# Optimization experiments

Hardware: AMD Instinct MI355X
Metric: run time of the kernel (lower is better)

The kernel has to match this reference:

```python
import jax, jax.numpy as jnp
import numpy as np

B, N, C, H, P, K = 32, 4096, 64, 256, 8, 2


def setup_inputs() -> dict:
    key = jax.random.key(0)
    k1, k2, k3, k4 = jax.random.split(key, 4)
    s1 = 1.0 / np.sqrt(C)
    s2 = 1.0 / np.sqrt(H)
    return {
        "u_t": jax.random.normal(k1, (B, N, C), dtype=jnp.float32),
        "W1": jax.random.normal(k2, (P, C, H), dtype=jnp.float32) * s1,
        "b1": jnp.zeros((P, H), dtype=jnp.float32),
        "W2": jax.random.normal(k3, (P, H, C), dtype=jnp.float32) * s2,
        "b2": jnp.zeros((P, C), dtype=jnp.float32),
        "Wr": jax.random.normal(k4, (C, P), dtype=jnp.float32) * s1,
        "br": jnp.zeros((P,), dtype=jnp.float32),
        "top_k": K,
    }


def reference(u_t, W1, b1, W2, b2, Wr, br, top_k):
    # u_state = u_t[..., :output_channels]; here C_in == output_channels
    u_state = u_t
    # Router: mean-pool over spatial points -> per-sample logits over primitives
    pooled = jnp.mean(u_state, axis=1)                     # (B, C)
    logits = pooled @ Wr + br                              # (B, P)
    topk_vals, topk_idx = jax.lax.top_k(logits, top_k)     # (B, K)
    w = jax.nn.softmax(topk_vals, axis=-1)                 # (B, K) combine weights
    # Sparse dispatch: gather only the selected experts' params per sample
    W1e = W1[topk_idx]                                     # (B, K, C, H)
    b1e = b1[topk_idx]                                     # (B, K, H)
    W2e = W2[topk_idx]                                     # (B, K, H, C)
    b2e = b2[topk_idx]                                     # (B, K, C)
    # Primitive operator: pointwise 2-layer GELU MLP (erf gelu, torch default)
    h1 = jax.nn.gelu(jnp.einsum('bnc,bkch->bknh', u_t, W1e) + b1e[:, :, None, :],
                     approximate=False)                    # (B, K, N, H)
    delta = jnp.einsum('bknh,bkhc->bknc', h1, W2e) + b2e[:, :, None, :]  # (B, K, N, C)
    # Weighted combine: delta_sum = sum_k w_k * delta_k
    delta_sum = jnp.einsum('bknc,bk->bnc', delta, w)       # (B, N, C)
    return u_state + delta_sum
```

## Files before the change

### kernel.cpp

```cpp
#include <hip/hip_runtime.h>
#include <hip/hip_bf16.h>
#include <math.h>

#define B_ 32
#define N_ 4096
#define C_ 64
#define H_ 256
#define P_ 8
#define NPOOL 1024

typedef short bf16x8 __attribute__((ext_vector_type(8)));
typedef float f32x4 __attribute__((ext_vector_type(4)));

union BF8 { bf16x8 v; unsigned int w[4]; };

__device__ __forceinline__ unsigned short f2bf(float f) {
    union { float f; unsigned int u; } v; v.f = f;
    unsigned int r = v.u + 0x7FFFu + ((v.u >> 16) & 1u);
    return (unsigned short)(r >> 16);
}
__device__ __forceinline__ float bf2f(unsigned short h) {
    union { float f; unsigned int u; } v; v.u = ((unsigned int)h) << 16; return v.f;
}
__device__ __forceinline__ unsigned int pk_bf16(float lo, float hi) {
    unsigned int r;
    asm("v_cvt_pk_bf16_f32 %0, %1, %2" : "=v"(r) : "v"(lo), "v"(hi));
    return r;
}
__device__ __forceinline__ float gelu_w(float x, float wk) {
    float x2 = x * x;
    float y2 = x * fmaf(0.10294322f, x2, 2.30220772f);
    float e  = __builtin_amdgcn_exp2f(y2);
    float rc = __builtin_amdgcn_rcpf(e + 1.0f);
    float wx = wk * x;
    return fmaf(-wx, rc, wx);
}
__device__ __forceinline__ int hperm_p(int p) {
    int t = p >> 4, d = p & 15;
    return ((t >> 1) << 5) + ((d >> 2) << 3) + ((t & 1) << 2) + (d & 3);
}

__global__ void prep_pool(const float* __restrict__ W1, const float* __restrict__ W2,
                          const float* __restrict__ b1, const float* __restrict__ u,
                          const float* __restrict__ Wr, const float* __restrict__ br,
                          unsigned short* __restrict__ W1P, unsigned short* __restrict__ W2T,
                          unsigned short* __restrict__ b1P, float* __restrict__ pooled,
                          int* __restrict__ counter, float4* __restrict__ route) {
    __shared__ union {
        unsigned short t[256 * 66];
        unsigned short s[64 * 258];
        struct { float red[4][64]; float lgAll[B_][P_]; } pr;
    } sh;
    __shared__ int isLast;

    const int bid = blockIdx.x, tid = threadIdx.x;

    if (bid < 16) {
        const int e = bid >> 1, m = bid & 1;
        if (m == 0) {
            const float* src = W1 + (e << 14);
            #pragma unroll
            for (int i = 0; i < 16; ++i) {
                int c = i * 4 + (tid >> 6), h4 = (tid & 63) * 4;
                float4 v = *(const float4*)(src + c * 256 + h4);
                sh.t[(h4 + 0) * 66 + c] = f2bf(v.x);
                sh.t[(h4 + 1) * 66 + c] = f2bf(v.y);
                sh.t[(h4 + 2) * 66 + c] = f2bf(v.z);
                sh.t[(h4 + 3) * 66 + c] = f2bf(v.w);
            }
            __syncthreads();
            unsigned short* dst = W1P + (e << 14);
            #pragma unroll
            for (int i = 0; i < 32; ++i) {
                int p = i * 8 + (tid >> 5), c2 = (tid & 31) * 2;
                int h = hperm_p(p);
                *(ushort2*)(dst + (p << 6) + c2) = *(const ushort2*)&sh.t[h * 66 + c2];
            }
        } else {
            const float* src = W2 + (e << 14);
            #pragma unroll
            for (int i = 0; i < 16; ++i) {
                int h = i * 16 + (tid >> 4), c4 = (tid & 15) * 4;
                float4 v = *(const float4*)(src + (h << 6) + c4);
                sh.s[(c4 + 0) * 258 + h] = f2bf(v.x);
                sh.s[(c4 + 1) * 258 + h] = f2bf(v.y);
                sh.s[(c4 + 2) * 258 + h] = f2bf(v.z);
                sh.s[(c4 + 3) * 258 + h] = f2bf(v.w);
            }
            __syncthreads();
            unsigned short* dst = W2T + (e << 14);
            #pragma unroll
            for (int i = 0; i < 32; ++i) {
                int c = i * 2 + (tid >> 7), h2 = (tid & 127) * 2;
                *(ushort2*)(dst + (c << 8) + h2) = *(const ushort2*)&sh.s[c * 258 + h2];
            }
        }
        return;
    }
    if (bid == 16) {
        #pragma unroll
        for (int i = 0; i < 8; ++i) {
            int oi = i * 256 + tid;
            int e = oi >> 8, p = oi & 255;
            b1P[oi] = f2bf(b1[(e << 8) + hperm_p(p)]);
        }
        return;
    }
    int pb = bid - 17;
    int b = pb >> 5, chunk = pb & 31;
    int c = tid & 63, rg = tid >> 6;
    const float* base = u + ((size_t)b * N_ + (size_t)chunk * 128) * C_;
    float s = 0.f;
    #pragma unroll 4
    for (int i = 0; i < 32; ++i) s += base[(i * 4 + rg) * C_ + c];
    sh.pr.red[rg][c] = s;
    __syncthreads();
    if (tid < 64) {
        float t4 = sh.pr.red[0][tid] + sh.pr.red[1][tid] + sh.pr.red[2][tid] + sh.pr.red[3][tid];
        atomicAdd(&pooled[b * C_ + tid], t4);
        __threadfence();
    }
    __syncthreads();
    if (tid == 0) {
        int old = atomicAdd(counter, 1);
        isLast = (old == NPOOL - 1);
    }
    __syncthreads();
    if (!isLast) return;
    __threadfence();
    {
        int rb = tid >> 3, p = tid & 7;
        const float* pb2 = pooled + rb * C_;
        float sacc = br[p];
        #pragma unroll
        for (int cc = 0; cc < C_; ++cc) {
            float pv = __hip_atomic_load(&pb2[cc], __ATOMIC_RELAXED, __HIP_MEMORY_SCOPE_AGENT);
            sacc += pv * (1.0f / N_) * Wr[cc * P_ + p];
        }
        sh.pr.lgAll[rb][p] = sacc;
    }
    __syncthreads();
    if (tid < B_) {
        float lg[P_];
        #pragma unroll
        for (int p = 0; p < P_; ++p) lg[p] = sh.pr.lgAll[tid][p];
        int i0 = 0;
        #pragma unroll
        for (int p = 1; p < P_; ++p) if (lg[p] > lg[i0]) i0 = p;
        int i1 = (i0 == 0) ? 1 : 0;
        #pragma unroll
        for (int p = 0; p < P_; ++p) if (p != i0 && lg[p] > lg[i1]) i1 = p;
        float e1 = __expf(lg[i1] - lg[i0]);
        float w0 = 1.f / (1.f + e1);
        route[tid] = make_float4(w0, e1 * w0, __int_as_float(i0), __int_as_float(i1));
    }
}

__device__ __forceinline__ void comp_tp(const bf16x8 (&A)[2][2], const bf16x8 (&Bw)[4],
                                        ushort4 bva, ushort4 bvb, float wk,
                                        const bf16x8 (&ub)[4][2], f32x4 (&acc2)[4][4]) {
    f32x4 c1[2][4];
    #pragma unroll
    for (int tt = 0; tt < 2; ++tt)
        #pragma unroll
        for (int rt = 0; rt < 4; ++rt)
            #pragma unroll
            for (int q = 0; q < 4; ++q) c1[tt][rt][q] = 0.f;
    #pragma unroll
    for (int ks = 0; ks < 2; ++ks)
        #pragma unroll
        for (int tt = 0; tt < 2; ++tt)
            #pragma unroll
            for (int rt = 0; rt < 4; ++rt)
                c1[tt][rt] = __builtin_amdgcn_mfma_f32_16x16x32_bf16(A[tt][ks], ub[rt][ks], c1[tt][rt], 0, 0, 0);
    float bv[8];
    bv[0] = bf2f(bva.x); bv[1] = bf2f(bva.y); bv[2] = bf2f(bva.z); bv[3] = bf2f(bva.w);
    bv[4] = bf2f(bvb.x); bv[5] = bf2f(bvb.y); bv[6] = bf2f(bvb.z); bv[7] = bf2f(bvb.w);
    #pragma unroll
    for (int rt = 0; rt < 4; ++rt) {
        float gv[8];
        #pragma unroll
        for (int j = 0; j < 4; ++j) {
            gv[j]     = gelu_w(c1[0][rt][j] + bv[j],     wk);
            gv[4 + j] = gelu_w(c1[1][rt][j] + bv[4 + j], wk);
        }
        BF8 t;
        t.w[0] = pk_bf16(gv[0], gv[1]); t.w[1] = pk_bf16(gv[2], gv[3]);
        t.w[2] = pk_bf16(gv[4], gv[5]); t.w[3] = pk_bf16(gv[6], gv[7]);
        bf16x8 a2 = t.v;
        #pragma unroll
        for (int ct = 0; ct < 4; ++ct)
            acc2[ct][rt] = __builtin_amdgcn_mfma_f32_16x16x32_bf16(a2, Bw[ct], acc2[ct][rt], 0, 0, 0);
    }
}

#define LOADS(A, Bw, bva, bvb, tp) \
    A[0][0] = *(const bf16x8*)(w1p + (((tp) * 32 +  0 + r) << 6) +  0 + g * 8); \
    A[0][1] = *(const bf16x8*)(w1p + (((tp) * 32 +  0 + r) << 6) + 32 + g * 8); \
    A[1][0] = *(const bf16x8*)(w1p + (((tp) * 32 + 16 + r) << 6) +  0 + g * 8); \
    A[1][1] = *(const bf16x8*)(w1p + (((tp) * 32 + 16 + r) << 6) + 32 + g * 8); \
    Bw[0] = *(const bf16x8*)(w2t + (( 0 + r) << 8) + (tp) * 32 + g * 8); \
    Bw[1] = *(const bf16x8*)(w2t + ((16 + r) << 8) + (tp) * 32 + g * 8); \
    Bw[2] = *(const bf16x8*)(w2t + ((32 + r) << 8) + (tp) * 32 + g * 8); \
    Bw[3] = *(const bf16x8*)(w2t + ((48 + r) << 8) + (tp) * 32 + g * 8); \
    bva = *(const ushort4*)(b1e + (tp) * 32 + 4 * g); \
    bvb = *(const ushort4*)(b1e + (tp) * 32 + 16 + 4 * g);

__global__ __launch_bounds__(256, 2)
void moe_main(const float* __restrict__ u, const unsigned short* __restrict__ W1P,
              const unsigned short* __restrict__ W2T, const unsigned short* __restrict__ b1P,
              const float* __restrict__ b2, const float4* __restrict__ route,
              float* __restrict__ out) {
    const int tid = threadIdx.x;
    const int wv = tid >> 6, lane = tid & 63;
    const int r = lane & 15, g = lane >> 4;
    const int b = blockIdx.x >> 4;
    const int nslab = ((blockIdx.x & 15) << 2) + wv;
    const int n0 = nslab << 6;

    float4 rd = route[b];

    const float* ubase = u + ((size_t)b * N_ + n0) * C_;
    bf16x8 ub[4][2];
    #pragma unroll
    for (int rt = 0; rt < 4; ++rt) {
        const float* rp = ubase + (rt * 16 + r) * C_;
        #pragma unroll
        for (int ks = 0; ks < 2; ++ks) {
            float4 lo = *(const float4*)(rp + ks * 32 + g * 8);
            float4 hi = *(const float4*)(rp + ks * 32 + g * 8 + 4);
            BF8 t;
            t.w[0] = pk_bf16(lo.x, lo.y); t.w[1] = pk_bf16(lo.z, lo.w);
            t.w[2] = pk_bf16(hi.x, hi.y); t.w[3] = pk_bf16(hi.z, hi.w);
            ub[rt][ks] = t.v;
        }
    }

    f32x4 acc2[4][4];
    #pragma unroll
    for (int ct = 0; ct < 4; ++ct)
        #pragma unroll
        for (int rt = 0; rt < 4; ++rt)
            #pragma unroll
            for (int q = 0; q < 4; ++q) acc2[ct][rt][q] = 0.f;

    #pragma unroll
    for (int ke = 0; ke < 2; ++ke) {
        const int e = ke ? __float_as_int(rd.w) : __float_as_int(rd.z);
        const float wk = ke ? rd.y : rd.x;
        const unsigned short* w1p = W1P + (e << 14);
        const unsigned short* w2t = W2T + (e << 14);
        const unsigned short* b1e = b1P + (e << 8);

        bf16x8 Aa[2][2], Ba[4]; ushort4 va0, va1;
        bf16x8 Ab[2][2], Bb[4]; ushort4 vb0, vb1;
        LOADS(Aa, Ba, va0, va1, 0)
        #pragma unroll
        for (int tpp = 0; tpp < 4; ++tpp) {
            LOADS(Ab, Bb, vb0, vb1, 2 * tpp + 1)
            comp_tp(Aa, Ba, va0, va1, wk, ub, acc2);
            if (tpp < 3) { LOADS(Aa, Ba, va0, va1, 2 * tpp + 2) }
            comp_tp(Ab, Bb, vb0, vb1, wk, ub, acc2);
        }
    }

    const int e0 = __float_as_int(rd.z), e1i = __float_as_int(rd.w);
    float bsum[4];
    #pragma unroll
    for (int ct = 0; ct < 4; ++ct) {
        int c = ct * 16 + r;
        bsum[ct] = rd.x * b2[e0 * C_ + c] + rd.y * b2[e1i * C_ + c];
    }
    float* obase = out + ((size_t)b * N_ + n0) * C_;
    #pragma unroll
    for (int rt = 0; rt < 4; ++rt)
        #pragma unroll
        for (int j = 0; j < 4; ++j) {
            int row = rt * 16 + 4 * g + j;
            #pragma unroll
            for (int ct = 0; ct < 4; ++ct) {
                int c = ct * 16 + r;
                obase[row * C_ + c] = ubase[row * C_ + c] + acc2[ct][rt][j] + bsum[ct];
            }
        }
}

extern "C" void kernel_launch(void* const* d_in, const int* in_sizes, int n_in,
                              void* d_out, int out_size, void* d_ws, size_t ws_size,
                              hipStream_t stream) {
    const float* u  = (const float*)d_in[0];
    const float* W1 = (const float*)d_in[1];
    const float* b1 = (const float*)d_in[2];
    const float* W2 = (const float*)d_in[3];
    const float* b2 = (const float*)d_in[4];
    const float* Wr = (const float*)d_in[5];
    const float* br = (const float*)d_in[6];
    float* out = (float*)d_out;

    char* ws = (char*)d_ws;
    float* pooled        = (float*)ws;
    int* counter         = (int*)(ws + 8192);
    float4* route        = (float4*)(ws + 8256);
    unsigned short* b1P  = (unsigned short*)(ws + 8768);
    unsigned short* W1P  = (unsigned short*)(ws + 16384);
    unsigned short* W2T  = (unsigned short*)(ws + 16384 + 262144);

    hipMemsetAsync(ws, 0, 8256, stream);
    prep_pool<<<1041, 256, 0, stream>>>(W1, W2, b1, u, Wr, br, W1P, W2T, b1P, pooled, counter, route);
    moe_main<<<512, 256, 0, stream>>>(u, W1P, W2T, b1P, b2, route, out);
}
```

Baseline: 171.3 us.

## Stage expert weights into LDS via direct global-to-LDS loads in fragment layout

The prep kernel now writes each expert's W1, W2 and b1 into one contiguous block already laid out in MFMA fragment order, folding the separate bias block into the weight-conversion blocks. The main kernel copies the selected expert's block into shared memory with global_load_lds and reads fragments from LDS instead of issuing per-wave global loads. The b1 bias is folded into the MFMA accumulator initialisation. This removes the four-fold redundant global and L2 weight traffic across waves, but adds about 64KB of LDS per block, which may limit occupancy to two blocks per CU. It also adds block-wide barriers and removes the register double-buffered prefetch overlap.

```diff
diff --git a/kernel.cpp b/kernel.cpp
--- a/kernel.cpp
+++ b/kernel.cpp
@@ -8,11 +8,12 @@
 #define H_ 256
 #define P_ 8
 #define NPOOL 1024
+#define EBLK 66048
 
 typedef short bf16x8 __attribute__((ext_vector_type(8)));
 typedef float f32x4 __attribute__((ext_vector_type(4)));
 
-union BF8 { bf16x8 v; unsigned int w[4]; };
+union BF8 { bf16x8 v; unsigned int w[4]; unsigned short h[8]; };
 
 __device__ __forceinline__ unsigned short f2bf(float f) {
     union { float f; unsigned int u; } v; v.f = f;
@@ -39,12 +40,16 @@
     int t = p >> 4, d = p & 15;
     return ((t >> 1) << 5) + ((d >> 2) << 3) + ((t & 1) << 2) + (d & 3);
 }
+__device__ __forceinline__ void gload16(const void* g, void* l) {
+    __builtin_amdgcn_global_load_lds(
+        (const __attribute__((address_space(1))) unsigned int*)g,
+        (__attribute__((address_space(3))) unsigned int*)l, 16, 0, 0);
+}
 
 __global__ void prep_pool(const float* __restrict__ W1, const float* __restrict__ W2,
                           const float* __restrict__ b1, const float* __restrict__ u,
                           const float* __restrict__ Wr, const float* __restrict__ br,
-                          unsigned short* __restrict__ W1P, unsigned short* __restrict__ W2T,
-                          unsigned short* __restrict__ b1P, float* __restrict__ pooled,
+                          unsigned short* __restrict__ WL, float* __restrict__ pooled,
                           int* __restrict__ counter, float4* __restrict__ route) {
     __shared__ union {
         unsigned short t[256 * 66];
@@ -57,6 +62,7 @@
 
     if (bid < 16) {
         const int e = bid >> 1, m = bid & 1;
+        unsigned short* dstW = WL + (size_t)e * (EBLK / 2);
         if (m == 0) {
             const float* src = W1 + (e << 14);
             #pragma unroll
@@ -69,12 +75,24 @@
                 sh.t[(h4 + 3) * 66 + c] = f2bf(v.w);
             }
             __syncthreads();
-            unsigned short* dst = W1P + (e << 14);
-            #pragma unroll
-            for (int i = 0; i < 32; ++i) {
-                int p = i * 8 + (tid >> 5), c2 = (tid & 31) * 2;
-                int h = hperm_p(p);
-                *(ushort2*)(dst + (p << 6) + c2) = *(const ushort2*)&sh.t[h * 66 + c2];
+            #pragma unroll
+            for (int i = 0; i < 8; ++i) {
+                int idx = i * 256 + tid;
+                int fid = idx >> 6, ln = idx & 63;
+                int tp = fid >> 2, tt = (fid >> 1) & 1, ks = fid & 1;
+                int rr = ln & 15, gg = ln >> 4;
+                const unsigned short* sp = &sh.t[hperm_p(tp * 32 + tt * 16 + rr) * 66 + ks * 32 + gg * 8];
+                BF8 o;
+                #pragma unroll
+                for (int mm = 0; mm < 8; ++mm) o.h[mm] = sp[mm];
+                *(bf16x8*)(dstW + ((fid * 64 + ln) << 3)) = o.v;
+            }
+            if (tid < 32) {
+                BF8 o;
+                #pragma unroll
+                for (int mm = 0; mm < 8; ++mm)
+                    o.h[mm] = f2bf(b1[(e << 8) + hperm_p(tid * 8 + mm)]);
+                *(bf16x8*)(dstW + 32768 + (tid << 3)) = o.v;
             }
         } else {
             const float* src = W2 + (e << 14);
@@ -88,25 +106,22 @@
                 sh.s[(c4 + 3) * 258 + h] = f2bf(v.w);
             }
             __syncthreads();
-            unsigned short* dst = W2T + (e << 14);
-            #pragma unroll
-            for (int i = 0; i < 32; ++i) {
-                int c = i * 2 + (tid >> 7), h2 = (tid & 127) * 2;
-                *(ushort2*)(dst + (c << 8) + h2) = *(const ushort2*)&sh.s[c * 258 + h2];
+            #pragma unroll
+            for (int i = 0; i < 8; ++i) {
+                int idx = i * 256 + tid;
+                int fid = idx >> 6, ln = idx & 63;
+                int tp = fid >> 2, ct = fid & 3;
+                int rr = ln & 15, gg = ln >> 4;
+                const unsigned short* sp = &sh.s[(ct * 16 + rr) * 258 + tp * 32 + gg * 8];
+                BF8 o;
+                #pragma unroll
+                for (int mm = 0; mm < 8; ++mm) o.h[mm] = sp[mm];
+                *(bf16x8*)(dstW + 16384 + ((fid * 64 + ln) << 3)) = o.v;
             }
         }
         return;
     }
-    if (bid == 16) {
-        #pragma unroll
-        for (int i = 0; i < 8; ++i) {
-            int oi = i * 256 + tid;
-            int e = oi >> 8, p = oi & 255;
-            b1P[oi] = f2bf(b1[(e << 8) + hperm_p(p)]);
-        }
-        return;
-    }
-    int pb = bid - 17;
+    int pb = bid - 16;
     int b = pb >> 5, chunk = pb & 31;
     int c = tid & 63, rg = tid >> 6;
     const float* base = u + ((size_t)b * N_ + (size_t)chunk * 128) * C_;
@@ -159,30 +174,30 @@
 __device__ __forceinline__ void comp_tp(const bf16x8 (&A)[2][2], const bf16x8 (&Bw)[4],
                                         ushort4 bva, ushort4 bvb, float wk,
                                         const bf16x8 (&ub)[4][2], f32x4 (&acc2)[4][4]) {
-    f32x4 c1[2][4];
-    #pragma unroll
-    for (int tt = 0; tt < 2; ++tt)
-        #pragma unroll
-        for (int rt = 0; rt < 4; ++rt)
-            #pragma unroll
-            for (int q = 0; q < 4; ++q) c1[tt][rt][q] = 0.f;
-    #pragma unroll
-    for (int ks = 0; ks < 2; ++ks)
-        #pragma unroll
-        for (int tt = 0; tt < 2; ++tt)
-            #pragma unroll
-            for (int rt = 0; rt < 4; ++rt)
-                c1[tt][rt] = __builtin_amdgcn_mfma_f32_16x16x32_bf16(A[tt][ks], ub[rt][ks], c1[tt][rt], 0, 0, 0);
     float bv[8];
     bv[0] = bf2f(bva.x); bv[1] = bf2f(bva.y); bv[2] = bf2f(bva.z); bv[3] = bf2f(bva.w);
     bv[4] = bf2f(bvb.x); bv[5] = bf2f(bvb.y); bv[6] = bf2f(bvb.z); bv[7] = bf2f(bvb.w);
+    f32x4 c1[2][4];
+    #pragma unroll
+    for (int tt = 0; tt < 2; ++tt)
+        #pragma unroll
+        for (int rt = 0; rt < 4; ++rt)
+            #pragma unroll
+            for (int q = 0; q < 4; ++q) c1[tt][rt][q] = bv[tt * 4 + q];
+    #pragma unroll
+    for (int ks = 0; ks < 2; ++ks)
+        #pragma unroll
+        for (int tt = 0; tt < 2; ++tt)
+            #pragma unroll
+            for (int rt = 0; rt < 4; ++rt)
+                c1[tt][rt] = __builtin_amdgcn_mfma_f32_16x16x32_bf16(A[tt][ks], ub[rt][ks], c1[tt][rt], 0, 0, 0);
     #pragma unroll
     for (int rt = 0; rt < 4; ++rt) {
         float gv[8];
         #pragma unroll
         for (int j = 0; j < 4; ++j) {
-            gv[j]     = gelu_w(c1[0][rt][j] + bv[j],     wk);
-            gv[4 + j] = gelu_w(c1[1][rt][j] + bv[4 + j], wk);
+            gv[j]     = gelu_w(c1[0][rt][j], wk);
+            gv[4 + j] = gelu_w(c1[1][rt][j], wk);
         }
         BF8 t;
         t.w[0] = pk_bf16(gv[0], gv[1]); t.w[1] = pk_bf16(gv[2], gv[3]);
@@ -194,29 +209,18 @@
     }
 }
 
-#define LOADS(A, Bw, bva, bvb, tp) \
-    A[0][0] = *(const bf16x8*)(w1p + (((tp) * 32 +  0 + r) << 6) +  0 + g * 8); \
-    A[0][1] = *(const bf16x8*)(w1p + (((tp) * 32 +  0 + r) << 6) + 32 + g * 8); \
-    A[1][0] = *(const bf16x8*)(w1p + (((tp) * 32 + 16 + r) << 6) +  0 + g * 8); \
-    A[1][1] = *(const bf16x8*)(w1p + (((tp) * 32 + 16 + r) << 6) + 32 + g * 8); \
-    Bw[0] = *(const bf16x8*)(w2t + (( 0 + r) << 8) + (tp) * 32 + g * 8); \
-    Bw[1] = *(const bf16x8*)(w2t + ((16 + r) << 8) + (tp) * 32 + g * 8); \
-    Bw[2] = *(const bf16x8*)(w2t + ((32 + r) << 8) + (tp) * 32 + g * 8); \
-    Bw[3] = *(const bf16x8*)(w2t + ((48 + r) << 8) + (tp) * 32 + g * 8); \
-    bva = *(const ushort4*)(b1e + (tp) * 32 + 4 * g); \
-    bvb = *(const ushort4*)(b1e + (tp) * 32 + 16 + 4 * g);
-
 __global__ __launch_bounds__(256, 2)
-void moe_main(const float* __restrict__ u, const unsigned short* __restrict__ W1P,
-              const unsigned short* __restrict__ W2T, const unsigned short* __restrict__ b1P,
+void moe_main(const float* __restrict__ u, const unsigned short* __restrict__ WL,
               const float* __restrict__ b2, const float4* __restrict__ route,
               float* __restrict__ out) {
+    __shared__ __align__(16) unsigned char wlds[EBLK];
+
     const int tid = threadIdx.x;
     const int wv = tid >> 6, lane = tid & 63;
     const int r = lane & 15, g = lane >> 4;
+    const int lbyte = lane * 16;
     const int b = blockIdx.x >> 4;
-    const int nslab = ((blockIdx.x & 15) << 2) + wv;
-    const int n0 = nslab << 6;
+    const int n0 = (((blockIdx.x & 15) << 2) + wv) << 6;
 
     float4 rd = route[b];
 
@@ -244,23 +248,33 @@
             #pragma unroll
             for (int q = 0; q < 4; ++q) acc2[ct][rt][q] = 0.f;
 
-    #pragma unroll
     for (int ke = 0; ke < 2; ++ke) {
         const int e = ke ? __float_as_int(rd.w) : __float_as_int(rd.z);
         const float wk = ke ? rd.y : rd.x;
-        const unsigned short* w1p = W1P + (e << 14);
-        const unsigned short* w2t = W2T + (e << 14);
-        const unsigned short* b1e = b1P + (e << 8);
-
-        bf16x8 Aa[2][2], Ba[4]; ushort4 va0, va1;
-        bf16x8 Ab[2][2], Bb[4]; ushort4 vb0, vb1;
-        LOADS(Aa, Ba, va0, va1, 0)
-        #pragma unroll
-        for (int tpp = 0; tpp < 4; ++tpp) {
-            LOADS(Ab, Bb, vb0, vb1, 2 * tpp + 1)
-            comp_tp(Aa, Ba, va0, va1, wk, ub, acc2);
-            if (tpp < 3) { LOADS(Aa, Ba, va0, va1, 2 * tpp + 2) }
-            comp_tp(Ab, Bb, vb0, vb1, wk, ub, acc2);
+
+        if (ke) __syncthreads();
+        const char* wsrc = (const char*)WL + (size_t)e * EBLK;
+        #pragma unroll
+        for (int i2 = 0; i2 < 16; ++i2)
+            gload16(wsrc + i2 * 4096 + wv * 1024 + lbyte, &wlds[i2 * 4096 + wv * 1024]);
+        if (tid < 32)
+            gload16(wsrc + 65536 + lbyte, &wlds[65536]);
+        __syncthreads();
+
+        #pragma unroll
+        for (int tp = 0; tp < 8; ++tp) {
+            bf16x8 A[2][2], Bw[4];
+            #pragma unroll
+            for (int tt = 0; tt < 2; ++tt)
+                #pragma unroll
+                for (int ks = 0; ks < 2; ++ks)
+                    A[tt][ks] = *(const bf16x8*)&wlds[((tp * 4 + tt * 2 + ks) << 10) + lbyte];
+            #pragma unroll
+            for (int ct = 0; ct < 4; ++ct)
+                Bw[ct] = *(const bf16x8*)&wlds[32768 + ((tp * 4 + ct) << 10) + lbyte];
+            ushort4 bva = *(const ushort4*)&wlds[65536 + tp * 64 + g * 8];
+            ushort4 bvb = *(const ushort4*)&wlds[65536 + tp * 64 + 32 + g * 8];
+            comp_tp(A, Bw, bva, bvb, wk, ub, acc2);
         }
     }
 
@@ -298,14 +312,12 @@
     float* out = (float*)d_out;
 
     char* ws = (char*)d_ws;
-    float* pooled        = (float*)ws;
-    int* counter         = (int*)(ws + 8192);
-    float4* route        = (float4*)(ws + 8256);
-    unsigned short* b1P  = (unsigned short*)(ws + 8768);
-    unsigned short* W1P  = (unsigned short*)(ws + 16384);
-    unsigned short* W2T  = (unsigned short*)(ws + 16384 + 262144);
+    float* pooled       = (float*)ws;
+    int* counter        = (int*)(ws + 8192);
+    float4* route       = (float4*)(ws + 8256);
+    unsigned short* WL  = (unsigned short*)(ws + 16384);
 
     hipMemsetAsync(ws, 0, 8256, stream);
-    prep_pool<<<1041, 256, 0, stream>>>(W1, W2, b1, u, Wr, br, W1P, W2T, b1P, pooled, counter, route);
-    moe_main<<<512, 256, 0, stream>>>(u, W1P, W2T, b1P, b2, route, out);
-}
+    prep_pool<<<1040, 256, 0, stream>>>(W1, W2, b1, u, Wr, br, WL, pooled, counter, route);
+    moe_main<<<512, 256, 0, stream>>>(u, WL, b2, route, out);
+}
```

Result: faster. 160.1 us (-6.5%).
